# Kernel tuning notes

Measured on AMD Instinct MI355X. Metric: run time of the kernel, lower is better.

## Reference

```python
import jax, jax.numpy as jnp
import numpy as np

N_NODES = 100000
FEAT = 256      # input_size == out_size (required for multi-layer consistency in original code)
OUT = 256
B = 20000       # batch of target nodes
S = 25          # sampled neighbors per node (padded)


def setup_inputs() -> dict:
    key = jax.random.key(0)
    k1, k2, k3, k4, k5, k6 = jax.random.split(key, 6)
    feats = jax.random.normal(k1, (N_NODES, FEAT), dtype=jnp.float32)
    nodes = jax.random.randint(k2, (B,), 0, N_NODES)
    samp_neighs = jax.random.randint(k3, (B, S), 0, N_NODES)
    val_lens = jax.random.randint(k4, (B,), 1, S + 1)  # at least 1 valid neighbor
    # xavier_uniform-like scale for [out, 2*in] weights
    s0 = (6.0 / (OUT + 2 * FEAT)) ** 0.5
    s1 = (6.0 / (OUT + 2 * OUT)) ** 0.5
    w0 = jax.random.uniform(k5, (OUT, 2 * FEAT), jnp.float32, -s0, s0)
    w1 = jax.random.uniform(k6, (OUT, 2 * OUT), jnp.float32, -s1, s1)
    return {"feats": feats, "nodes": nodes, "samp_neighs": samp_neighs,
            "val_lens": val_lens, "w0": w0, "w1": w1}


def _mean_agg(neigh_feats, val_lens):
    # neigh_feats: [B, S, F]; ragged MEAN over first val_lens[b] neighbors
    mask = (jnp.arange(neigh_feats.shape[1])[None, :] < val_lens[:, None]).astype(neigh_feats.dtype)
    summed = jnp.einsum('bsf,bs->bf', neigh_feats, mask)
    return summed / val_lens[:, None].astype(neigh_feats.dtype)


def reference(feats, nodes, samp_neighs, val_lens, w0, w1):
    self_raw = feats[nodes]           # [B, F] gather
    neigh = feats[samp_neighs]        # [B, S, F] gather
    agg = _mean_agg(neigh, val_lens)  # [B, F]
    feat_data = self_raw
    for w in (w0, w1):
        # SageLayer: relu(W @ concat(self, agg).T).T == relu(concat @ W.T)
        combined = jnp.concatenate([self_raw, agg], axis=1)  # [B, 2F]
        feat_data = jax.nn.relu(combined @ w.T)              # [B, OUT]
        # Original recomputes aggregator with feat_data as self_feats, but MEAN
        # aggregation (gcn=False) depends only on raw neighbor feats -> identical.
        agg = _mean_agg(neigh, val_lens)
    return feat_data
```

## Files before the change

### kernel.cpp

```cpp
#include <hip/hip_runtime.h>

typedef unsigned short u16;
typedef unsigned int   u32;

#define NB     20000
#define SNB    25
#define FEAT   256
#define K2     512
#define OUTF   256

#define BM     32
#define NPW    8
#define LDA    520
#define BK     32
#define LDB    40
#define NCHUNK (K2 / BK)

typedef __attribute__((ext_vector_type(8))) short short8;
typedef __attribute__((ext_vector_type(4))) float f32x4;

__device__ __forceinline__ u32 f2bf(float f) {
  union { u32 i; float f; } x; x.f = f;
  return (x.i + 0x7fffu + ((x.i >> 16) & 1u)) >> 16;
}
__device__ __forceinline__ u32 pack2(float a, float b) {
  return f2bf(a) | (f2bf(b) << 16);
}

__global__ __launch_bounds__(256) void convw_kernel(
    const float* __restrict__ w_raw, u16* __restrict__ w_bf) {
  const int i = blockIdx.x * 256 + threadIdx.x;
  w_bf[i] = (u16)f2bf(w_raw[i]);
}

__global__ __launch_bounds__(256) void fused_kernel(
    const float* __restrict__ feats, const int* __restrict__ nodes,
    const int* __restrict__ neighs, const int* __restrict__ lens,
    const u16* __restrict__ W, float* __restrict__ C) {
  __shared__ u16 As[BM * LDA];
  __shared__ u16 Bs[OUTF * LDB];

  const int tid   = threadIdx.x;
  const int wave  = tid >> 6;
  const int lane  = tid & 63;
  const int mbase = blockIdx.x * BM;

  {
    const uint4* src = (const uint4*)(W + (size_t)tid * K2);
    uint4* dst = (uint4*)&Bs[tid * LDB];
#pragma unroll
    for (int c = 0; c < 4; ++c) dst[c] = src[c];
  }

  for (int p = 0; p < NPW; ++p) {
    const int m = wave * NPW + p;
    const int b = mbase + m;
    const int self = nodes[b];
    const int len  = lens[b];
    int myidx = (lane < SNB) ? neighs[b * SNB + lane] : 0;

    const float4 sv = ((const float4*)(feats + (size_t)self * FEAT))[lane];

    float4 a0 = {0.f, 0.f, 0.f, 0.f}, a1 = a0, a2 = a0, a3 = a0;
    int s = 0;
    for (; s + 4 <= len; s += 4) {
      const int i0 = __shfl(myidx, s);
      const int i1 = __shfl(myidx, s + 1);
      const int i2 = __shfl(myidx, s + 2);
      const int i3 = __shfl(myidx, s + 3);
      const float4 v0 = ((const float4*)(feats + (size_t)i0 * FEAT))[lane];
      const float4 v1 = ((const float4*)(feats + (size_t)i1 * FEAT))[lane];
      const float4 v2 = ((const float4*)(feats + (size_t)i2 * FEAT))[lane];
      const float4 v3 = ((const float4*)(feats + (size_t)i3 * FEAT))[lane];
      a0.x += v0.x; a0.y += v0.y; a0.z += v0.z; a0.w += v0.w;
      a1.x += v1.x; a1.y += v1.y; a1.z += v1.z; a1.w += v1.w;
      a2.x += v2.x; a2.y += v2.y; a2.z += v2.z; a2.w += v2.w;
      a3.x += v3.x; a3.y += v3.y; a3.z += v3.z; a3.w += v3.w;
    }
    for (; s < len; ++s) {
      const int i0 = __shfl(myidx, s);
      const float4 v0 = ((const float4*)(feats + (size_t)i0 * FEAT))[lane];
      a0.x += v0.x; a0.y += v0.y; a0.z += v0.z; a0.w += v0.w;
    }
    const float inv = 1.f / (float)len;
    const float m0 = (a0.x + a1.x + a2.x + a3.x) * inv;
    const float m1 = (a0.y + a1.y + a2.y + a3.y) * inv;
    const float m2 = (a0.z + a1.z + a2.z + a3.z) * inv;
    const float m3 = (a0.w + a1.w + a2.w + a3.w) * inv;

    uint2* arow = (uint2*)&As[m * LDA];
    uint2 pe; pe.x = pack2(sv.x, sv.y); pe.y = pack2(sv.z, sv.w);
    arow[lane] = pe;
    uint2 pm; pm.x = pack2(m0, m1); pm.y = pack2(m2, m3);
    arow[64 + lane] = pm;
  }
  __syncthreads();

  const int wc  = wave * 64;
  const int r16 = lane & 15;
  const int kq  = (lane >> 4) * 8;

  f32x4 acc[2][4] = {};

  for (int kc = 0; ; ) {
    const int k0 = kc * BK;
    short8 af[2], bf[4];
#pragma unroll
    for (int i = 0; i < 2; ++i)
      af[i] = *(const short8*)&As[(i * 16 + r16) * LDA + k0 + kq];
#pragma unroll
    for (int j = 0; j < 4; ++j)
      bf[j] = *(const short8*)&Bs[(wc + j * 16 + r16) * LDB + kq];

#pragma unroll
    for (int i = 0; i < 2; ++i)
#pragma unroll
      for (int j = 0; j < 4; ++j)
        acc[i][j] = __builtin_amdgcn_mfma_f32_16x16x32_bf16(af[i], bf[j],
                                                            acc[i][j], 0, 0, 0);
    if (++kc == NCHUNK) break;
    __syncthreads();
    {
      const uint4* src = (const uint4*)(W + (size_t)tid * K2 + kc * BK);
      uint4* dst = (uint4*)&Bs[tid * LDB];
#pragma unroll
      for (int c = 0; c < 4; ++c) dst[c] = src[c];
    }
    __syncthreads();
  }

#pragma unroll
  for (int i = 0; i < 2; ++i)
#pragma unroll
    for (int r = 0; r < 4; ++r) {
      const int row = mbase + i * 16 + (lane >> 4) * 4 + r;
#pragma unroll
      for (int j = 0; j < 4; ++j) {
        const int col = wc + j * 16 + (lane & 15);
        const float v = acc[i][j][r];
        C[(size_t)row * OUTF + col] = v > 0.f ? v : 0.f;
      }
    }
}

extern "C" void kernel_launch(void* const* d_in, const int* in_sizes, int n_in,
                              void* d_out, int out_size, void* d_ws, size_t ws_size,
                              hipStream_t stream) {
  const float* feats = (const float*)d_in[0];
  const int* nodes   = (const int*)d_in[1];
  const int* neighs  = (const int*)d_in[2];
  const int* lens    = (const int*)d_in[3];
  const float* w1    = (const float*)d_in[5];
  float* out = (float*)d_out;

  u16* w1bf = (u16*)d_ws;

  convw_kernel<<<512, 256, 0, stream>>>(w1, w1bf);
  fused_kernel<<<NB / BM, 256, 0, stream>>>(feats, nodes, neighs, lens, w1bf, out);
}
```

Measured before the change: 205.7 us.

## Halve block rows and read weight fragments directly from global memory

The block tile shrinks from 32 to 16 rows, doubling the grid to 1250 blocks for more parallelism in the gather phase. The shared-memory staging of the bf16 weight chunks and the per-chunk barriers are removed, and each wave now loads its B fragments straight from global memory (the 256 KB bf16 weight should stay cache-resident). This cuts LDS traffic and synchronisation, but each block now rereads the whole weight matrix and only 16 rows share each weight fetch.

```diff
diff --git a/kernel.cpp b/kernel.cpp
--- a/kernel.cpp
+++ b/kernel.cpp
@@ -9,11 +9,10 @@
 #define K2     512
 #define OUTF   256
 
-#define BM     32
-#define NPW    8
+#define BM     16
+#define NPW    4
 #define LDA    520
 #define BK     32
-#define LDB    40
 #define NCHUNK (K2 / BK)
 
 typedef __attribute__((ext_vector_type(8))) short short8;
@@ -38,19 +37,11 @@
     const int* __restrict__ neighs, const int* __restrict__ lens,
     const u16* __restrict__ W, float* __restrict__ C) {
   __shared__ u16 As[BM * LDA];
-  __shared__ u16 Bs[OUTF * LDB];
 
   const int tid   = threadIdx.x;
   const int wave  = tid >> 6;
   const int lane  = tid & 63;
   const int mbase = blockIdx.x * BM;
-
-  {
-    const uint4* src = (const uint4*)(W + (size_t)tid * K2);
-    uint4* dst = (uint4*)&Bs[tid * LDB];
-#pragma unroll
-    for (int c = 0; c < 4; ++c) dst[c] = src[c];
-  }
 
   for (int p = 0; p < NPW; ++p) {
     const int m = wave * NPW + p;
@@ -100,47 +91,30 @@
   const int r16 = lane & 15;
   const int kq  = (lane >> 4) * 8;
 
-  f32x4 acc[2][4] = {};
-
-  for (int kc = 0; ; ) {
-    const int k0 = kc * BK;
-    short8 af[2], bf[4];
-#pragma unroll
-    for (int i = 0; i < 2; ++i)
-      af[i] = *(const short8*)&As[(i * 16 + r16) * LDA + k0 + kq];
-#pragma unroll
-    for (int j = 0; j < 4; ++j)
-      bf[j] = *(const short8*)&Bs[(wc + j * 16 + r16) * LDB + kq];
+  f32x4 acc[4] = {};
 
 #pragma unroll
-    for (int i = 0; i < 2; ++i)
+  for (int kc = 0; kc < NCHUNK; ++kc) {
+    const int k0 = kc * BK;
+    const short8 af = *(const short8*)&As[r16 * LDA + k0 + kq];
 #pragma unroll
-      for (int j = 0; j < 4; ++j)
-        acc[i][j] = __builtin_amdgcn_mfma_f32_16x16x32_bf16(af[i], bf[j],
-                                                            acc[i][j], 0, 0, 0);
-    if (++kc == NCHUNK) break;
-    __syncthreads();
-    {
-      const uint4* src = (const uint4*)(W + (size_t)tid * K2 + kc * BK);
-      uint4* dst = (uint4*)&Bs[tid * LDB];
-#pragma unroll
-      for (int c = 0; c < 4; ++c) dst[c] = src[c];
+    for (int j = 0; j < 4; ++j) {
+      const short8 bf =
+          *(const short8*)&W[(size_t)(wc + j * 16 + r16) * K2 + k0 + kq];
+      acc[j] = __builtin_amdgcn_mfma_f32_16x16x32_bf16(af, bf, acc[j], 0, 0, 0);
     }
-    __syncthreads();
   }
 
 #pragma unroll
-  for (int i = 0; i < 2; ++i)
+  for (int r = 0; r < 4; ++r) {
+    const int row = mbase + (lane >> 4) * 4 + r;
 #pragma unroll
-    for (int r = 0; r < 4; ++r) {
-      const int row = mbase + i * 16 + (lane >> 4) * 4 + r;
-#pragma unroll
-      for (int j = 0; j < 4; ++j) {
-        const int col = wc + j * 16 + (lane & 15);
-        const float v = acc[i][j][r];
-        C[(size_t)row * OUTF + col] = v > 0.f ? v : 0.f;
-      }
+    for (int j = 0; j < 4; ++j) {
+      const int col = wc + j * 16 + r16;
+      const float v = acc[j][r];
+      C[(size_t)row * OUTF + col] = v > 0.f ? v : 0.f;
     }
+  }
 }
 
 extern "C" void kernel_launch(void* const* d_in, const int* in_sizes, int n_in,
```

Measured after the change: 215.0 us. 4.5% more time.
